# Performance work log

Measured on AMD Instinct MI355X. Metric: run time of the kernel, lower is better.

## Reference

```python
import jax, jax.numpy as jnp
import numpy as np

NEG_BIG = -1e10  # K.switch(A==0, -1e10, 0) mask value
LRELU_ALPHA = 0.2


def setup_inputs() -> dict:
    key = jax.random.key(0)
    kX, kA, kW, kS, kN = jax.random.split(key, 5)
    B, N, F, H, F_ = 4, 2048, 256, 8, 64
    X = jax.random.normal(kX, (B, N, F), dtype=jnp.float32)
    A = jax.random.bernoulli(kA, 0.05, (B, N, N)).astype(jnp.float32)
    eye = jnp.eye(N, dtype=jnp.float32)[None]
    A = jnp.maximum(A, eye)
    W = jax.random.normal(kW, (H, F, F_), dtype=jnp.float32) * 0.05
    a_self = jax.random.normal(kS, (H, F_), dtype=jnp.float32) * 0.05
    a_neigh = jax.random.normal(kN, (H, F_), dtype=jnp.float32) * 0.05
    return {"X": X, "A": A, "W": W, "a_self": a_self, "a_neigh": a_neigh}


def reference(X, A, W, a_self, a_neigh):
    # per-head linear transform, vectorized over heads: [B,H,N,F_]
    h = jnp.einsum('bnf,hfo->bhno', X, W)
    att_s = jnp.einsum('bhno,ho->bhn', h, a_self)    # attn_for_self
    att_n = jnp.einsum('bhno,ho->bhn', h, a_neigh)   # attn_for_neighs
    # broadcast-add -> dense NxN scores per head, LeakyReLU(0.2)
    dense = att_s[:, :, :, None] + att_n[:, :, None, :]          # [B,H,N,N]
    dense = jax.nn.leaky_relu(dense, LRELU_ALPHA)
    mask = jnp.where(A == 0.0, NEG_BIG, 0.0)[:, None, :, :]      # [B,1,N,N]
    attn = jax.nn.softmax(dense + mask, axis=-1)
    # weighted aggregation (dropout is identity at inference / attn_dropout=0)
    out = jnp.einsum('bhnm,bhmo->bhno', attn, h)                 # [B,H,N,F_]
    out = jax.nn.relu(out)                                       # per-head activation (concat mode)
    B, H, N, F_ = out.shape
    return out.transpose(0, 2, 1, 3).reshape(B, N, H * F_)       # concat heads
```

## Files before the change

kernel.cpp:

```cpp
#include <hip/hip_runtime.h>


constexpr int GN  = 2048;
constexpr int GHF = 512;

using sh8    = __attribute__((ext_vector_type(8))) short;
using us4g   = __attribute__((ext_vector_type(4))) unsigned short;
using f32x4g = __attribute__((ext_vector_type(4))) float;
using u32x4g = __attribute__((ext_vector_type(4))) unsigned int;
using i32x4g = __attribute__((ext_vector_type(4))) int;

__device__ inline float gat_bf2f(unsigned short u) {
    union { unsigned int i; float f; } c; c.i = ((unsigned int)u) << 16; return c.f;
}
__device__ inline unsigned short gat_f2bf(float f) {
    union { float f; unsigned int i; } c; c.f = f;
    return (unsigned short)((c.i + 0x7fffu + ((c.i >> 16) & 1u)) >> 16);
}
__device__ inline int gat_isf32(const float* __restrict__ Aw) {
    float a = Aw[0];
    return (a == 0.0f) || (a == 1.0f);
}
__device__ inline unsigned int gat_enc(float f) {
    union { float f; unsigned int u; } c; c.f = f;
    return (c.u & 0x80000000u) ? ~c.u : (c.u | 0x80000000u);
}
__device__ inline float gat_dec(unsigned int e) {
    union { float f; unsigned int u; } c;
    c.u = (e & 0x80000000u) ? (e & 0x7fffffffu) : ~e;
    return c.f;
}
__device__ inline size_t gat_hswz_idx(int o, int j) {
    int jc = j >> 5, quad = (j >> 3) & 3, e = j & 7;
    int lane = quad * 16 + (o & 15);
    return (((size_t)(jc * 4 + (o >> 4))) * 64 + lane) * 8 + e;
}
__device__ inline size_t gat_wf_idx(int hh, int k, int col) {
    int kg = k >> 5, quad = (k >> 3) & 3, e = k & 7;
    int ct = col >> 4, lrw = col & 15;
    return ((((size_t)hh * 8 + kg) * 4 + ct) * 64 + (quad * 16 + lrw)) * 8 + e;
}

__global__ void GraphAttention_62981400429165_kernel() {}

constexpr size_t OFF_HS   = 256;
constexpr size_t OFF_ATTS = OFF_HS   + 8388608;
constexpr size_t OFF_TB   = OFF_ATTS + 262144;
constexpr size_t OFF_MASK = OFF_TB   + 262144;
constexpr size_t OFF_MAXN = OFF_MASK + 2097152;
constexpr size_t OFF_XC   = OFF_MAXN + 256;
constexpr size_t OFF_WC   = OFF_XC   + 4194304;

__global__ __launch_bounds__(256) void k_mask_conv(const void* __restrict__ Araw,
                                                   const void* __restrict__ Xraw,
                                                   const void* __restrict__ Wraw,
                                                   unsigned long long* __restrict__ mask,
                                                   unsigned int* __restrict__ maxn_enc,
                                                   unsigned short* __restrict__ Xc,
                                                   unsigned short* __restrict__ Wf) {
    int tid = threadIdx.x, blk = blockIdx.x;
    int isf = gat_isf32((const float*)Araw);
    if (blk < 8192) {
        if (blk == 0 && tid < 32) maxn_enc[tid] = 0u;
        size_t i8 = ((size_t)blk * 256 + tid) * 8;
        unsigned int byte = 0;
        if (isf) {
            f32x4g v0 = *(const f32x4g*)((const float*)Araw + i8);
            f32x4g v1 = *(const f32x4g*)((const float*)Araw + i8 + 4);
#pragma unroll
            for (int e = 0; e < 4; e++) {
                byte |= (v0[e] != 0.0f ? 1u : 0u) << e;
                byte |= (v1[e] != 0.0f ? 1u : 0u) << (e + 4);
            }
        } else {
            u32x4g v = *(const u32x4g*)((const unsigned short*)Araw + i8);
#pragma unroll
            for (int w = 0; w < 4; w++) {
                byte |= ((v[w] & 0xffffu) != 0u ? 1u : 0u) << (2 * w);
                byte |= ((v[w] >> 16) != 0u ? 1u : 0u) << (2 * w + 1);
            }
        }
        ((unsigned char*)mask)[i8 >> 3] = (unsigned char)byte;
    } else if (blk < 9216) {
        size_t i8 = ((size_t)(blk - 8192) * 256 + tid) * 8;
        if (isf) {
            f32x4g v0 = *(const f32x4g*)((const float*)Xraw + i8);
            f32x4g v1 = *(const f32x4g*)((const float*)Xraw + i8 + 4);
            us4g lo, hi;
#pragma unroll
            for (int e = 0; e < 4; e++) { lo[e] = gat_f2bf(v0[e]); hi[e] = gat_f2bf(v1[e]); }
            *(us4g*)&Xc[i8]     = lo;
            *(us4g*)&Xc[i8 + 4] = hi;
        } else {
            *(u32x4g*)&Xc[i8] = *(const u32x4g*)((const unsigned short*)Xraw + i8);
        }
    } else {
        int gid = (blk - 9216) * 256 + tid;
        int lane = gid & 63, ct = (gid >> 6) & 3, kg = (gid >> 8) & 7, hh = gid >> 11;
        int quad = lane >> 4, lrw = lane & 15;
        int col = ct * 16 + lrw;
        us4g lo, hi;
#pragma unroll
        for (int e = 0; e < 8; e++) {
            int k = kg * 32 + quad * 8 + e;
            size_t src = (size_t)hh * 16384 + (size_t)k * 64 + col;
            unsigned short v = isf ? gat_f2bf(((const float*)Wraw)[src])
                                   : ((const unsigned short*)Wraw)[src];
            if (e < 4) lo[e] = v; else hi[e - 4] = v;
        }
        *(us4g*)&Wf[(size_t)gid * 8]     = lo;
        *(us4g*)&Wf[(size_t)gid * 8 + 4] = hi;
    }
}

constexpr int LDW = 264;
__global__ __launch_bounds__(256) void k_gemm1(const unsigned short* __restrict__ Xc,
                                               const unsigned short* __restrict__ Wf,
                                               const void* __restrict__ aSraw,
                                               const void* __restrict__ aNraw,
                                               const float* __restrict__ Aw,
                                               unsigned short* __restrict__ hswz,
                                               float* __restrict__ att_s,
                                               unsigned int* __restrict__ Tb,
                                               unsigned int* __restrict__ maxn_enc) {
    int blk = blockIdx.x;
    int bh = blk >> 5, it = blk & 31;
    int b = bh >> 3, hh = bh & 7;
    int isf = gat_isf32(Aw);
#if defined(__gfx950__)
    __shared__ unsigned short CtT[64 * LDW];
    int wave = threadIdx.x >> 6, lane = threadIdx.x & 63;
    int lrw = lane & 15, quad = lane >> 4;
    int row0 = it * 64 + wave * 16;
    const unsigned short* wfh = Wf + (size_t)hh * 16384 + lane * 8;
    f32x4g acc[4] = {};
#pragma unroll 2
    for (int kg = 0; kg < 8; kg++) {
        sh8 a = *(const sh8*)&Xc[((size_t)(b * GN) + row0 + lrw) * 256 + kg * 32 + quad * 8];
        const unsigned short* wp = wfh + kg * 2048;
        sh8 w0 = *(const sh8*)&wp[0];
        sh8 w1 = *(const sh8*)&wp[512];
        sh8 w2 = *(const sh8*)&wp[1024];
        sh8 w3 = *(const sh8*)&wp[1536];
        acc[0] = __builtin_amdgcn_mfma_f32_16x16x32_bf16(a, w0, acc[0], 0, 0, 0);
        acc[1] = __builtin_amdgcn_mfma_f32_16x16x32_bf16(a, w1, acc[1], 0, 0, 0);
        acc[2] = __builtin_amdgcn_mfma_f32_16x16x32_bf16(a, w2, acc[2], 0, 0, 0);
        acc[3] = __builtin_amdgcn_mfma_f32_16x16x32_bf16(a, w3, acc[3], 0, 0, 0);
    }
    float as_l[4], an_l[4];
#pragma unroll
    for (int ct = 0; ct < 4; ct++) {
        int col = hh * 64 + ct * 16 + lrw;
        as_l[ct] = isf ? ((const float*)aSraw)[col] : gat_bf2f(((const unsigned short*)aSraw)[col]);
        an_l[ct] = isf ? ((const float*)aNraw)[col] : gat_bf2f(((const unsigned short*)aNraw)[col]);
    }
    float wmax = -3e38f;
#pragma unroll
    for (int r = 0; r < 4; r++) {
        float ps = acc[0][r] * as_l[0] + acc[1][r] * as_l[1]
                 + acc[2][r] * as_l[2] + acc[3][r] * as_l[3];
        float pn = acc[0][r] * an_l[0] + acc[1][r] * an_l[1]
                 + acc[2][r] * an_l[2] + acc[3][r] * an_l[3];
        for (int off = 1; off < 16; off <<= 1) {
            ps += __shfl_xor(ps, off);
            pn += __shfl_xor(pn, off);
        }
        int row = row0 + quad * 4 + r;
        if (lrw == 0) {
            att_s[bh * GN + row] = ps;
            Tb[bh * GN + row] = ((unsigned int)gat_f2bf(__expf(pn)) << 16)
                              | (unsigned int)gat_f2bf(__expf(0.2f * pn));
        }
        wmax = fmaxf(wmax, pn);
    }
    wmax = fmaxf(wmax, __shfl_xor(wmax, 16));
    wmax = fmaxf(wmax, __shfl_xor(wmax, 32));
    if (lane == 0) atomicMax(&maxn_enc[bh], gat_enc(wmax));
#pragma unroll
    for (int ct = 0; ct < 4; ct++) {
        int o = ct * 16 + lrw;
        int nloc = wave * 16 + quad * 4;
        us4g v;
        v[0] = gat_f2bf(acc[ct][0]);
        v[1] = gat_f2bf(acc[ct][1]);
        v[2] = gat_f2bf(acc[ct][2]);
        v[3] = gat_f2bf(acc[ct][3]);
        *(us4g*)&CtT[o * LDW + nloc] = v;
    }
    __syncthreads();
#pragma unroll
    for (int k = 0; k < 2; k++) {
        int id = k * 256 + threadIdx.x;
        int ln = id & 63, t = id >> 6;
        int jc_loc = t >> 2, ct = t & 3;
        int lrw2 = ln & 15, quad2 = ln >> 4;
        int o = ct * 16 + lrw2;
        int nloc = jc_loc * 32 + quad2 * 8;
        sh8 v = *(const sh8*)&CtT[o * LDW + nloc];
        size_t dst = ((((size_t)(bh * 64 + it * 2 + jc_loc)) * 4 + ct) * 64 + ln) * 8;
        *(sh8*)&hswz[dst] = v;
    }
#else
    if (threadIdx.x < 64) {
        int row = it * 64 + threadIdx.x;
        float hrow[64];
        for (int col = 0; col < 64; col++) {
            float sacc = 0.f;
            for (int k = 0; k < 256; k++)
                sacc += gat_bf2f(Xc[((size_t)(b * GN) + row) * 256 + k])
                      * gat_bf2f(Wf[gat_wf_idx(hh, k, col)]);
            hrow[col] = sacc;
        }
        size_t base = (size_t)bh * 64 * GN;
        for (int col = 0; col < 64; col++)
            hswz[base + gat_hswz_idx(col, row)] = gat_f2bf(hrow[col]);
        float ps = 0.f, pn = 0.f;
        for (int col = 0; col < 64; col++) {
            float as = isf ? ((const float*)aSraw)[hh * 64 + col] : gat_bf2f(((const unsigned short*)aSraw)[hh * 64 + col]);
            float an = isf ? ((const float*)aNraw)[hh * 64 + col] : gat_bf2f(((const unsigned short*)aNraw)[hh * 64 + col]);
            ps += hrow[col] * as;
            pn += hrow[col] * an;
        }
        att_s[bh * GN + row] = ps;
        Tb[bh * GN + row] = ((unsigned int)gat_f2bf(__expf(pn)) << 16)
                          | (unsigned int)gat_f2bf(__expf(0.2f * pn));
        atomicMax(&maxn_enc[bh], gat_enc(pn));
    }
#endif
}

__global__ __launch_bounds__(256, 4) void k_attn_av(const unsigned int* __restrict__ mask32,
                                                    const unsigned short* __restrict__ hswz,
                                                    const float* __restrict__ att_s,
                                                    const unsigned int* __restrict__ Tb,
                                                    const unsigned int* __restrict__ maxn_enc,
                                                    const float* __restrict__ Aw,
                                                    void* __restrict__ outv) {
    int blk = blockIdx.x;
    int bh = blk & 31, it = blk >> 5;
    int b = bh >> 3, hh = bh & 7;
    int i0 = it * 32;
    int tid = threadIdx.x;
    int isf = gat_isf32(Aw);
    float maxn = gat_dec(maxn_enc[bh]);
    const unsigned int* Tp = Tb + (size_t)bh * GN;
#if defined(__gfx950__)
    int wave = tid >> 6, lane = tid & 63, lrw = lane & 15, quad = lane >> 4;
    int kq = quad * 8;
    int j0 = wave * 512;
    const unsigned short* hs = hswz + ((size_t)(bh * 64) + wave * 16) * 2048 + lane * 8;
    float k1[2], k2[2];
    const unsigned int* mrf[2];
    for (int f = 0; f < 2; f++) {
        int row = i0 + f * 16 + lrw;
        float s = att_s[bh * GN + row];
        float z = s + maxn;
        float c = fmaxf(z, 0.2f * z);
        k1[f] = __expf(s - c);
        k2[f] = __expf(0.2f * s - c);
        mrf[f] = mask32 + ((size_t)(b * GN) + row) * 64 + wave * 16;
    }
    f32x4g acc[2][4] = {};
    f32x4g accl[2] = {};
    sh8 ones;
#pragma unroll
    for (int e = 0; e < 8; e++) ones[e] = (short)0x3f80;

#pragma unroll 1
    for (int jg = 0; jg < 4; jg++) {
        u32x4g m0 = *(const u32x4g*)&mrf[0][jg * 4];
        u32x4g m1 = *(const u32x4g*)&mrf[1][jg * 4];
#pragma unroll
        for (int sj = 0; sj < 4; sj++) {
            int jc = jg * 4 + sj;
            int jq = j0 + jc * 32 + kq;
            u32x4g tA = *(const u32x4g*)&Tp[jq];
            u32x4g tB = *(const u32x4g*)&Tp[jq + 4];
            const unsigned short* hp = hs + jc * 2048;
            sh8 b0 = *(const sh8*)&hp[0];
            sh8 b1 = *(const sh8*)&hp[512];
            sh8 b2 = *(const sh8*)&hp[1024];
            sh8 b3 = *(const sh8*)&hp[1536];
            unsigned int w0 = m0[sj] >> kq;
            unsigned int w1 = m1[sj] >> kq;
            unsigned int q0[8], q1[8];
#pragma unroll
            for (int e = 0; e < 8; e++) {
                unsigned int word = (e < 4) ? tA[e] : tB[e - 4];
                float Ev  = __uint_as_float(word & 0xffff0000u);
                float E5v = __uint_as_float(word << 16);
                float p0 = fmaxf(k1[0] * Ev, k2[0] * E5v);
                float p1 = fmaxf(k1[1] * Ev, k2[1] * E5v);
                unsigned int s0 = (unsigned int)__builtin_amdgcn_sbfe((int)w0, (unsigned)e, 1u);
                unsigned int s1 = (unsigned int)__builtin_amdgcn_sbfe((int)w1, (unsigned)e, 1u);
                q0[e] = __float_as_uint(p0) & s0;
                q1[e] = __float_as_uint(p1) & s1;
            }
            i32x4g f0, f1;
#pragma unroll
            for (int pp = 0; pp < 4; pp++) {
                unsigned int r0, r1;
                asm("v_cvt_pk_bf16_f32 %0, %1, %2"
                    : "=v"(r0)
                    : "v"(__uint_as_float(q0[2 * pp])), "v"(__uint_as_float(q0[2 * pp + 1])));
                asm("v_cvt_pk_bf16_f32 %0, %1, %2"
                    : "=v"(r1)
                    : "v"(__uint_as_float(q1[2 * pp])), "v"(__uint_as_float(q1[2 * pp + 1])));
                f0[pp] = (int)r0;
                f1[pp] = (int)r1;
            }
            sh8 af0 = *(sh8*)&f0;
            sh8 af1 = *(sh8*)&f1;
            acc[0][0] = __builtin_amdgcn_mfma_f32_16x16x32_bf16(af0, b0, acc[0][0], 0, 0, 0);
            acc[1][0] = __builtin_amdgcn_mfma_f32_16x16x32_bf16(af1, b0, acc[1][0], 0, 0, 0);
            acc[0][1] = __builtin_amdgcn_mfma_f32_16x16x32_bf16(af0, b1, acc[0][1], 0, 0, 0);
            acc[1][1] = __builtin_amdgcn_mfma_f32_16x16x32_bf16(af1, b1, acc[1][1], 0, 0, 0);
            acc[0][2] = __builtin_amdgcn_mfma_f32_16x16x32_bf16(af0, b2, acc[0][2], 0, 0, 0);
            acc[1][2] = __builtin_amdgcn_mfma_f32_16x16x32_bf16(af1, b2, acc[1][2], 0, 0, 0);
            acc[0][3] = __builtin_amdgcn_mfma_f32_16x16x32_bf16(af0, b3, acc[0][3], 0, 0, 0);
            acc[1][3] = __builtin_amdgcn_mfma_f32_16x16x32_bf16(af1, b3, acc[1][3], 0, 0, 0);
            accl[0] = __builtin_amdgcn_mfma_f32_16x16x32_bf16(af0, ones, accl[0], 0, 0, 0);
            accl[1] = __builtin_amdgcn_mfma_f32_16x16x32_bf16(af1, ones, accl[1], 0, 0, 0);
        }
    }
    __shared__ float lred[4 * 32];
    __shared__ float lsum[32];
    __shared__ float red[4 * 2 * 16 * 17];
    if (lrw == 0) {
#pragma unroll
        for (int f = 0; f < 2; f++)
#pragma unroll
            for (int r = 0; r < 4; r++)
                lred[wave * 32 + f * 16 + quad * 4 + r] = accl[f][r];
    }
    __syncthreads();
    if (tid < 32)
        lsum[tid] = 1.0f / (lred[tid] + lred[32 + tid] + lred[64 + tid] + lred[96 + tid]);
    __syncthreads();
    for (int ct = 0; ct < 4; ct++) {
#pragma unroll
        for (int f = 0; f < 2; f++)
#pragma unroll
            for (int r = 0; r < 4; r++)
                red[wave * 544 + f * 272 + (quad * 4 + r) * 17 + lrw] = acc[f][ct][r];
        __syncthreads();
#pragma unroll
        for (int k = 0; k < 2; k++) {
            int pos = k * 256 + tid;
            int f = pos >> 8, r16 = (pos >> 4) & 15, c16 = pos & 15;
            int bse = f * 272 + r16 * 17 + c16;
            float sum = red[bse] + red[bse + 544] + red[bse + 1088] + red[bse + 1632];
            float v = sum * lsum[f * 16 + r16];
            v = v > 0.f ? v : 0.f;
            int row = i0 + f * 16 + r16;
            size_t o = ((size_t)(b * GN) + row) * GHF + hh * 64 + ct * 16 + c16;
            if (isf) ((float*)outv)[o] = v;
            else     ((unsigned short*)outv)[o] = gat_f2bf(v);
        }
        __syncthreads();
    }
#else
    int row = i0 + (tid >> 3), chh = (tid & 7) * 8;
    const unsigned short* hbb = hswz + (size_t)(bh * 64) * GN;
    const unsigned int* mr = mask32 + ((size_t)(b * GN) + row) * 64;
    float s = att_s[bh * GN + row];
    float z = s + maxn;
    float c = fmaxf(z, 0.2f * z);
    float k1 = __expf(s - c), k2 = __expf(0.2f * s - c);
    float l = 0.f;
    float accS[8] = {};
    for (int j = 0; j < GN; j++) {
        if (!((mr[j >> 5] >> (j & 31)) & 1u)) continue;
        unsigned int word = Tp[j];
        float Ev  = __uint_as_float(word & 0xffff0000u);
        float E5v = __uint_as_float(word << 16);
        float p = fmaxf(k1 * Ev, k2 * E5v);
        union { float f; unsigned int u; } t; t.f = p; t.u &= 0xffff0000u;
        l += t.f;
        for (int cc = 0; cc < 8; cc++)
            accS[cc] += t.f * gat_bf2f(hbb[gat_hswz_idx(chh + cc, j)]);
    }
    float li = 1.0f / l;
    for (int cc = 0; cc < 8; cc++) {
        float v = accS[cc] * li; v = v > 0.f ? v : 0.f;
        size_t oi = ((size_t)(b * GN) + row) * GHF + hh * 64 + chh + cc;
        if (isf) ((float*)outv)[oi] = v;
        else     ((unsigned short*)outv)[oi] = gat_f2bf(v);
    }
#endif
}

extern "C" void kernel_launch(void* const* d_in, const int* in_sizes, int n_in,
                              void* d_out, int out_size, void* d_ws, size_t ws_size,
                              hipStream_t stream) {
    const void* X  = d_in[0];
    const void* A  = d_in[1];
    const void* W  = d_in[2];
    const void* aS = d_in[3];
    const void* aN = d_in[4];

    char* ws = (char*)d_ws;
    unsigned short* hswz = (unsigned short*)(ws + OFF_HS);
    float* att_s = (float*)(ws + OFF_ATTS);
    unsigned int* Tb = (unsigned int*)(ws + OFF_TB);
    unsigned long long* mask = (unsigned long long*)(ws + OFF_MASK);
    unsigned int* maxn_enc = (unsigned int*)(ws + OFF_MAXN);
    unsigned short* Xc = (unsigned short*)(ws + OFF_XC);
    unsigned short* Wf = (unsigned short*)(ws + OFF_WC);

    k_mask_conv<<<9280, 256, 0, stream>>>(A, X, W, mask, maxn_enc, Xc, Wf);
    k_gemm1<<<1024, 256, 0, stream>>>(Xc, Wf, aS, aN, (const float*)A,
                                      hswz, att_s, Tb, maxn_enc);
    k_attn_av<<<2048, 256, 0, stream>>>((const unsigned int*)mask, hswz,
                                        att_s, Tb, maxn_enc,
                                        (const float*)A, d_out);
}
```

Measured before the change: 207.3 us.

## Switch attention path to fp16 packed math with 16-bit mask and fused X conversion

Replaces the bf16 probability path with fp16: exp terms are stored as separate fp16 arrays, probabilities are computed with packed v_pk_mul/max_f16 and masked with a precomputed 16-bit-per-element mask, and the AV matmul uses f16 MFMA. The bitmask becomes a 32MB halfword mask so no per-element bit extraction is needed. X conversion to bf16 is folded into the first GEMM, which removes a pass and a workspace buffer. The cost is far more mask traffic, 32MB against 2MB per call, and fp16 range limits handled by clamping pn to 10.

```diff
diff --git a/kernel.cpp b/kernel.cpp
--- a/kernel.cpp
+++ b/kernel.cpp
@@ -5,6 +5,7 @@
 constexpr int GHF = 512;
 
 using sh8    = __attribute__((ext_vector_type(8))) short;
+using hf8    = __attribute__((ext_vector_type(8))) _Float16;
 using us4g   = __attribute__((ext_vector_type(4))) unsigned short;
 using f32x4g = __attribute__((ext_vector_type(4))) float;
 using u32x4g = __attribute__((ext_vector_type(4))) unsigned int;
@@ -17,6 +18,13 @@
     union { float f; unsigned int i; } c; c.f = f;
     return (unsigned short)((c.i + 0x7fffu + ((c.i >> 16) & 1u)) >> 16);
 }
+__device__ inline unsigned short gat_f2h(float f) {
+    _Float16 h = (_Float16)f;
+    union { _Float16 h; unsigned short u; } c; c.h = h; return c.u;
+}
+__device__ inline float gat_h2f(unsigned short u) {
+    union { _Float16 h; unsigned short u; } c; c.u = u; return (float)c.h;
+}
 __device__ inline int gat_isf32(const float* __restrict__ Aw) {
     float a = Aw[0];
     return (a == 0.0f) || (a == 1.0f);
@@ -45,57 +53,41 @@
 
 constexpr size_t OFF_HS   = 256;
 constexpr size_t OFF_ATTS = OFF_HS   + 8388608;
-constexpr size_t OFF_TB   = OFF_ATTS + 262144;
-constexpr size_t OFF_MASK = OFF_TB   + 262144;
-constexpr size_t OFF_MAXN = OFF_MASK + 2097152;
-constexpr size_t OFF_XC   = OFF_MAXN + 256;
-constexpr size_t OFF_WC   = OFF_XC   + 4194304;
+constexpr size_t OFF_EF   = OFF_ATTS + 262144;
+constexpr size_t OFF_E5F  = OFF_EF   + 131072;
+constexpr size_t OFF_M16  = OFF_E5F  + 131072;
+constexpr size_t OFF_MAXN = OFF_M16  + 33554432;
+constexpr size_t OFF_WC   = OFF_MAXN + 256;
 
 __global__ __launch_bounds__(256) void k_mask_conv(const void* __restrict__ Araw,
-                                                   const void* __restrict__ Xraw,
                                                    const void* __restrict__ Wraw,
-                                                   unsigned long long* __restrict__ mask,
+                                                   unsigned short* __restrict__ M16,
                                                    unsigned int* __restrict__ maxn_enc,
-                                                   unsigned short* __restrict__ Xc,
                                                    unsigned short* __restrict__ Wf) {
     int tid = threadIdx.x, blk = blockIdx.x;
     int isf = gat_isf32((const float*)Araw);
     if (blk < 8192) {
         if (blk == 0 && tid < 32) maxn_enc[tid] = 0u;
         size_t i8 = ((size_t)blk * 256 + tid) * 8;
-        unsigned int byte = 0;
+        u32x4g mo;
         if (isf) {
             f32x4g v0 = *(const f32x4g*)((const float*)Araw + i8);
             f32x4g v1 = *(const f32x4g*)((const float*)Araw + i8 + 4);
-#pragma unroll
-            for (int e = 0; e < 4; e++) {
-                byte |= (v0[e] != 0.0f ? 1u : 0u) << e;
-                byte |= (v1[e] != 0.0f ? 1u : 0u) << (e + 4);
-            }
+            float el[8] = {v0[0], v0[1], v0[2], v0[3], v1[0], v1[1], v1[2], v1[3]};
+#pragma unroll
+            for (int p = 0; p < 4; p++)
+                mo[p] = (el[2 * p]     != 0.0f ? 0x0000FFFFu : 0u)
+                      | (el[2 * p + 1] != 0.0f ? 0xFFFF0000u : 0u);
         } else {
             u32x4g v = *(const u32x4g*)((const unsigned short*)Araw + i8);
 #pragma unroll
-            for (int w = 0; w < 4; w++) {
-                byte |= ((v[w] & 0xffffu) != 0u ? 1u : 0u) << (2 * w);
-                byte |= ((v[w] >> 16) != 0u ? 1u : 0u) << (2 * w + 1);
-            }
-        }
-        ((unsigned char*)mask)[i8 >> 3] = (unsigned char)byte;
-    } else if (blk < 9216) {
-        size_t i8 = ((size_t)(blk - 8192) * 256 + tid) * 8;
-        if (isf) {
-            f32x4g v0 = *(const f32x4g*)((const float*)Xraw + i8);
-            f32x4g v1 = *(const f32x4g*)((const float*)Xraw + i8 + 4);
-            us4g lo, hi;
-#pragma unroll
-            for (int e = 0; e < 4; e++) { lo[e] = gat_f2bf(v0[e]); hi[e] = gat_f2bf(v1[e]); }
-            *(us4g*)&Xc[i8]     = lo;
-            *(us4g*)&Xc[i8 + 4] = hi;
-        } else {
-            *(u32x4g*)&Xc[i8] = *(const u32x4g*)((const unsigned short*)Xraw + i8);
-        }
+            for (int p = 0; p < 4; p++)
+                mo[p] = ((v[p] & 0xffffu) != 0u ? 0x0000FFFFu : 0u)
+                      | ((v[p] >> 16)    != 0u ? 0xFFFF0000u : 0u);
+        }
+        *(u32x4g*)((unsigned int*)M16 + (i8 >> 1)) = mo;
     } else {
-        int gid = (blk - 9216) * 256 + tid;
+        int gid = (blk - 8192) * 256 + tid;
         int lane = gid & 63, ct = (gid >> 6) & 3, kg = (gid >> 8) & 7, hh = gid >> 11;
         int quad = lane >> 4, lrw = lane & 15;
         int col = ct * 16 + lrw;
@@ -114,14 +106,15 @@
 }
 
 constexpr int LDW = 264;
-__global__ __launch_bounds__(256) void k_gemm1(const unsigned short* __restrict__ Xc,
+__global__ __launch_bounds__(256) void k_gemm1(const void* __restrict__ Xraw,
                                                const unsigned short* __restrict__ Wf,
                                                const void* __restrict__ aSraw,
                                                const void* __restrict__ aNraw,
                                                const float* __restrict__ Aw,
                                                unsigned short* __restrict__ hswz,
                                                float* __restrict__ att_s,
-                                               unsigned int* __restrict__ Tb,
+                                               unsigned short* __restrict__ Ef,
+                                               unsigned short* __restrict__ E5f,
                                                unsigned int* __restrict__ maxn_enc) {
     int blk = blockIdx.x;
     int bh = blk >> 5, it = blk & 31;
@@ -133,10 +126,25 @@
     int lrw = lane & 15, quad = lane >> 4;
     int row0 = it * 64 + wave * 16;
     const unsigned short* wfh = Wf + (size_t)hh * 16384 + lane * 8;
+    size_t xbase = ((size_t)(b * GN) + row0 + lrw) * 256;
     f32x4g acc[4] = {};
 #pragma unroll 2
     for (int kg = 0; kg < 8; kg++) {
-        sh8 a = *(const sh8*)&Xc[((size_t)(b * GN) + row0 + lrw) * 256 + kg * 32 + quad * 8];
+        sh8 a;
+        if (isf) {
+            const float* xp = (const float*)Xraw + xbase + kg * 32 + quad * 8;
+            f32x4g x0 = *(const f32x4g*)xp;
+            f32x4g x1 = *(const f32x4g*)(xp + 4);
+            unsigned int w0_, w1_, w2_, w3_;
+            asm("v_cvt_pk_bf16_f32 %0, %1, %2" : "=v"(w0_) : "v"(x0[0]), "v"(x0[1]));
+            asm("v_cvt_pk_bf16_f32 %0, %1, %2" : "=v"(w1_) : "v"(x0[2]), "v"(x0[3]));
+            asm("v_cvt_pk_bf16_f32 %0, %1, %2" : "=v"(w2_) : "v"(x1[0]), "v"(x1[1]));
+            asm("v_cvt_pk_bf16_f32 %0, %1, %2" : "=v"(w3_) : "v"(x1[2]), "v"(x1[3]));
+            i32x4g aw = {(int)w0_, (int)w1_, (int)w2_, (int)w3_};
+            a = *(sh8*)&aw;
+        } else {
+            a = *(const sh8*)((const unsigned short*)Xraw + xbase + kg * 32 + quad * 8);
+        }
         const unsigned short* wp = wfh + kg * 2048;
         sh8 w0 = *(const sh8*)&wp[0];
         sh8 w1 = *(const sh8*)&wp[512];
@@ -168,8 +176,9 @@
         int row = row0 + quad * 4 + r;
         if (lrw == 0) {
             att_s[bh * GN + row] = ps;
-            Tb[bh * GN + row] = ((unsigned int)gat_f2bf(__expf(pn)) << 16)
-                              | (unsigned int)gat_f2bf(__expf(0.2f * pn));
+            float pnc = fminf(pn, 10.0f);
+            Ef[bh * GN + row]  = gat_f2h(__expf(pnc));
+            E5f[bh * GN + row] = gat_f2h(__expf(0.2f * pnc));
         }
         wmax = fmaxf(wmax, pn);
     }
@@ -181,10 +190,10 @@
         int o = ct * 16 + lrw;
         int nloc = wave * 16 + quad * 4;
         us4g v;
-        v[0] = gat_f2bf(acc[ct][0]);
-        v[1] = gat_f2bf(acc[ct][1]);
-        v[2] = gat_f2bf(acc[ct][2]);
-        v[3] = gat_f2bf(acc[ct][3]);
+        v[0] = gat_f2h(acc[ct][0]);
+        v[1] = gat_f2h(acc[ct][1]);
+        v[2] = gat_f2h(acc[ct][2]);
+        v[3] = gat_f2h(acc[ct][3]);
         *(us4g*)&CtT[o * LDW + nloc] = v;
     }
     __syncthreads();
@@ -206,14 +215,16 @@
         float hrow[64];
         for (int col = 0; col < 64; col++) {
             float sacc = 0.f;
-            for (int k = 0; k < 256; k++)
-                sacc += gat_bf2f(Xc[((size_t)(b * GN) + row) * 256 + k])
-                      * gat_bf2f(Wf[gat_wf_idx(hh, k, col)]);
+            for (int k = 0; k < 256; k++) {
+                float xv = isf ? ((const float*)Xraw)[((size_t)(b * GN) + row) * 256 + k]
+                               : gat_bf2f(((const unsigned short*)Xraw)[((size_t)(b * GN) + row) * 256 + k]);
+                sacc += xv * gat_bf2f(Wf[gat_wf_idx(hh, k, col)]);
+            }
             hrow[col] = sacc;
         }
         size_t base = (size_t)bh * 64 * GN;
         for (int col = 0; col < 64; col++)
-            hswz[base + gat_hswz_idx(col, row)] = gat_f2bf(hrow[col]);
+            hswz[base + gat_hswz_idx(col, row)] = gat_f2h(hrow[col]);
         float ps = 0.f, pn = 0.f;
         for (int col = 0; col < 64; col++) {
             float as = isf ? ((const float*)aSraw)[hh * 64 + col] : gat_bf2f(((const unsigned short*)aSraw)[hh * 64 + col]);
@@ -222,17 +233,19 @@
             pn += hrow[col] * an;
         }
         att_s[bh * GN + row] = ps;
-        Tb[bh * GN + row] = ((unsigned int)gat_f2bf(__expf(pn)) << 16)
-                          | (unsigned int)gat_f2bf(__expf(0.2f * pn));
+        float pnc = fminf(pn, 10.0f);
+        Ef[bh * GN + row]  = gat_f2h(__expf(pnc));
+        E5f[bh * GN + row] = gat_f2h(__expf(0.2f * pnc));
         atomicMax(&maxn_enc[bh], gat_enc(pn));
     }
 #endif
 }
 
-__global__ __launch_bounds__(256, 4) void k_attn_av(const unsigned int* __restrict__ mask32,
+__global__ __launch_bounds__(256, 4) void k_attn_av(const unsigned short* __restrict__ M16,
                                                     const unsigned short* __restrict__ hswz,
                                                     const float* __restrict__ att_s,
-                                                    const unsigned int* __restrict__ Tb,
+                                                    const unsigned short* __restrict__ Ef,
+                                                    const unsigned short* __restrict__ E5f,
                                                     const unsigned int* __restrict__ maxn_enc,
                                                     const float* __restrict__ Aw,
                                                     void* __restrict__ outv) {
@@ -243,85 +256,69 @@
     int tid = threadIdx.x;
     int isf = gat_isf32(Aw);
     float maxn = gat_dec(maxn_enc[bh]);
-    const unsigned int* Tp = Tb + (size_t)bh * GN;
 #if defined(__gfx950__)
     int wave = tid >> 6, lane = tid & 63, lrw = lane & 15, quad = lane >> 4;
-    int kq = quad * 8;
     int j0 = wave * 512;
     const unsigned short* hs = hswz + ((size_t)(bh * 64) + wave * 16) * 2048 + lane * 8;
-    float k1[2], k2[2];
-    const unsigned int* mrf[2];
+    const unsigned int* Eu  = (const unsigned int*)Ef  + (size_t)bh * 1024;
+    const unsigned int* E5u = (const unsigned int*)E5f + (size_t)bh * 1024;
+    unsigned int k1p[2], k2p[2];
+    const unsigned int* mrow[2];
     for (int f = 0; f < 2; f++) {
         int row = i0 + f * 16 + lrw;
         float s = att_s[bh * GN + row];
         float z = s + maxn;
         float c = fmaxf(z, 0.2f * z);
-        k1[f] = __expf(s - c);
-        k2[f] = __expf(0.2f * s - c);
-        mrf[f] = mask32 + ((size_t)(b * GN) + row) * 64 + wave * 16;
+        unsigned int u1 = gat_f2h(__expf(s - c));
+        unsigned int u2 = gat_f2h(__expf(0.2f * s - c));
+        k1p[f] = u1 * 0x00010001u;
+        k2p[f] = u2 * 0x00010001u;
+        mrow[f] = (const unsigned int*)M16 + ((size_t)(b * GN) + row) * 1024;
     }
     f32x4g acc[2][4] = {};
     f32x4g accl[2] = {};
-    sh8 ones;
-#pragma unroll
-    for (int e = 0; e < 8; e++) ones[e] = (short)0x3f80;
-
-#pragma unroll 1
-    for (int jg = 0; jg < 4; jg++) {
-        u32x4g m0 = *(const u32x4g*)&mrf[0][jg * 4];
-        u32x4g m1 = *(const u32x4g*)&mrf[1][jg * 4];
-#pragma unroll
-        for (int sj = 0; sj < 4; sj++) {
-            int jc = jg * 4 + sj;
-            int jq = j0 + jc * 32 + kq;
-            u32x4g tA = *(const u32x4g*)&Tp[jq];
-            u32x4g tB = *(const u32x4g*)&Tp[jq + 4];
-            const unsigned short* hp = hs + jc * 2048;
-            sh8 b0 = *(const sh8*)&hp[0];
-            sh8 b1 = *(const sh8*)&hp[512];
-            sh8 b2 = *(const sh8*)&hp[1024];
-            sh8 b3 = *(const sh8*)&hp[1536];
-            unsigned int w0 = m0[sj] >> kq;
-            unsigned int w1 = m1[sj] >> kq;
-            unsigned int q0[8], q1[8];
-#pragma unroll
-            for (int e = 0; e < 8; e++) {
-                unsigned int word = (e < 4) ? tA[e] : tB[e - 4];
-                float Ev  = __uint_as_float(word & 0xffff0000u);
-                float E5v = __uint_as_float(word << 16);
-                float p0 = fmaxf(k1[0] * Ev, k2[0] * E5v);
-                float p1 = fmaxf(k1[1] * Ev, k2[1] * E5v);
-                unsigned int s0 = (unsigned int)__builtin_amdgcn_sbfe((int)w0, (unsigned)e, 1u);
-                unsigned int s1 = (unsigned int)__builtin_amdgcn_sbfe((int)w1, (unsigned)e, 1u);
-                q0[e] = __float_as_uint(p0) & s0;
-                q1[e] = __float_as_uint(p1) & s1;
-            }
-            i32x4g f0, f1;
-#pragma unroll
-            for (int pp = 0; pp < 4; pp++) {
-                unsigned int r0, r1;
-                asm("v_cvt_pk_bf16_f32 %0, %1, %2"
-                    : "=v"(r0)
-                    : "v"(__uint_as_float(q0[2 * pp])), "v"(__uint_as_float(q0[2 * pp + 1])));
-                asm("v_cvt_pk_bf16_f32 %0, %1, %2"
-                    : "=v"(r1)
-                    : "v"(__uint_as_float(q1[2 * pp])), "v"(__uint_as_float(q1[2 * pp + 1])));
-                f0[pp] = (int)r0;
-                f1[pp] = (int)r1;
-            }
-            sh8 af0 = *(sh8*)&f0;
-            sh8 af1 = *(sh8*)&f1;
-            acc[0][0] = __builtin_amdgcn_mfma_f32_16x16x32_bf16(af0, b0, acc[0][0], 0, 0, 0);
-            acc[1][0] = __builtin_amdgcn_mfma_f32_16x16x32_bf16(af1, b0, acc[1][0], 0, 0, 0);
-            acc[0][1] = __builtin_amdgcn_mfma_f32_16x16x32_bf16(af0, b1, acc[0][1], 0, 0, 0);
-            acc[1][1] = __builtin_amdgcn_mfma_f32_16x16x32_bf16(af1, b1, acc[1][1], 0, 0, 0);
-            acc[0][2] = __builtin_amdgcn_mfma_f32_16x16x32_bf16(af0, b2, acc[0][2], 0, 0, 0);
-            acc[1][2] = __builtin_amdgcn_mfma_f32_16x16x32_bf16(af1, b2, acc[1][2], 0, 0, 0);
-            acc[0][3] = __builtin_amdgcn_mfma_f32_16x16x32_bf16(af0, b3, acc[0][3], 0, 0, 0);
-            acc[1][3] = __builtin_amdgcn_mfma_f32_16x16x32_bf16(af1, b3, acc[1][3], 0, 0, 0);
-            accl[0] = __builtin_amdgcn_mfma_f32_16x16x32_bf16(af0, ones, accl[0], 0, 0, 0);
-            accl[1] = __builtin_amdgcn_mfma_f32_16x16x32_bf16(af1, ones, accl[1], 0, 0, 0);
-        }
+    hf8 ones;
+#pragma unroll
+    for (int e = 0; e < 8; e++) ones[e] = (_Float16)1.0f;
+
+#pragma unroll 2
+    for (int jc = 0; jc < 16; jc++) {
+        int jh = ((j0 + jc * 32) >> 1) + quad * 4;
+        u32x4g Ep  = *(const u32x4g*)&Eu[jh];
+        u32x4g E5p = *(const u32x4g*)&E5u[jh];
+        u32x4g M0  = *(const u32x4g*)&mrow[0][jh];
+        u32x4g M1  = *(const u32x4g*)&mrow[1][jh];
+        const unsigned short* hp = hs + jc * 2048;
+        hf8 b0 = *(const hf8*)&hp[0];
+        hf8 b1 = *(const hf8*)&hp[512];
+        hf8 b2 = *(const hf8*)&hp[1024];
+        hf8 b3 = *(const hf8*)&hp[1536];
+        i32x4g f0, f1;
+#pragma unroll
+        for (int pp = 0; pp < 4; pp++) {
+            unsigned int a0, a1, m0w, a2, a3, m1w;
+            unsigned int ew = Ep[pp], e5w = E5p[pp];
+            asm("v_pk_mul_f16 %0, %1, %2" : "=v"(a0)  : "v"(k1p[0]), "v"(ew));
+            asm("v_pk_mul_f16 %0, %1, %2" : "=v"(a1)  : "v"(k2p[0]), "v"(e5w));
+            asm("v_pk_max_f16 %0, %1, %2" : "=v"(m0w) : "v"(a0), "v"(a1));
+            f0[pp] = (int)(m0w & M0[pp]);
+            asm("v_pk_mul_f16 %0, %1, %2" : "=v"(a2)  : "v"(k1p[1]), "v"(ew));
+            asm("v_pk_mul_f16 %0, %1, %2" : "=v"(a3)  : "v"(k2p[1]), "v"(e5w));
+            asm("v_pk_max_f16 %0, %1, %2" : "=v"(m1w) : "v"(a2), "v"(a3));
+            f1[pp] = (int)(m1w & M1[pp]);
+        }
+        hf8 af0 = *(hf8*)&f0;
+        hf8 af1 = *(hf8*)&f1;
+        acc[0][0] = __builtin_amdgcn_mfma_f32_16x16x32_f16(af0, b0, acc[0][0], 0, 0, 0);
+        acc[1][0] = __builtin_amdgcn_mfma_f32_16x16x32_f16(af1, b0, acc[1][0], 0, 0, 0);
+        acc[0][1] = __builtin_amdgcn_mfma_f32_16x16x32_f16(af0, b1, acc[0][1], 0, 0, 0);
+        acc[1][1] = __builtin_amdgcn_mfma_f32_16x16x32_f16(af1, b1, acc[1][1], 0, 0, 0);
+        acc[0][2] = __builtin_amdgcn_mfma_f32_16x16x32_f16(af0, b2, acc[0][2], 0, 0, 0);
+        acc[1][2] = __builtin_amdgcn_mfma_f32_16x16x32_f16(af1, b2, acc[1][2], 0, 0, 0);
+        acc[0][3] = __builtin_amdgcn_mfma_f32_16x16x32_f16(af0, b3, acc[0][3], 0, 0, 0);
+        acc[1][3] = __builtin_amdgcn_mfma_f32_16x16x32_f16(af1, b3, acc[1][3], 0, 0, 0);
+        accl[0] = __builtin_amdgcn_mfma_f32_16x16x32_f16(af0, ones, accl[0], 0, 0, 0);
+        accl[1] = __builtin_amdgcn_mfma_f32_16x16x32_f16(af1, ones, accl[1], 0, 0, 0);
     }
     __shared__ float lred[4 * 32];
     __shared__ float lsum[32];
@@ -362,7 +359,7 @@
 #else
     int row = i0 + (tid >> 3), chh = (tid & 7) * 8;
     const unsigned short* hbb = hswz + (size_t)(bh * 64) * GN;
-    const unsigned int* mr = mask32 + ((size_t)(b * GN) + row) * 64;
+    const unsigned short* mr = M16 + ((size_t)(b * GN) + row) * GN;
     float s = att_s[bh * GN + row];
     float z = s + maxn;
     float c = fmaxf(z, 0.2f * z);
@@ -370,15 +367,14 @@
     float l = 0.f;
     float accS[8] = {};
     for (int j = 0; j < GN; j++) {
-        if (!((mr[j >> 5] >> (j & 31)) & 1u)) continue;
-        unsigned int word = Tp[j];
-        float Ev  = __uint_as_float(word & 0xffff0000u);
-        float E5v = __uint_as_float(word << 16);
+        if (!mr[j]) continue;
+        float Ev  = gat_h2f(Ef[(size_t)bh * GN + j]);
+        float E5v = gat_h2f(E5f[(size_t)bh * GN + j]);
         float p = fmaxf(k1 * Ev, k2 * E5v);
-        union { float f; unsigned int u; } t; t.f = p; t.u &= 0xffff0000u;
-        l += t.f;
+        p = gat_h2f(gat_f2h(p));
+        l += p;
         for (int cc = 0; cc < 8; cc++)
-            accS[cc] += t.f * gat_bf2f(hbb[gat_hswz_idx(chh + cc, j)]);
+            accS[cc] += p * gat_h2f(hbb[gat_hswz_idx(chh + cc, j)]);
     }
     float li = 1.0f / l;
     for (int cc = 0; cc < 8; cc++) {
@@ -402,16 +398,15 @@
     char* ws = (char*)d_ws;
     unsigned short* hswz = (unsigned short*)(ws + OFF_HS);
     float* att_s = (float*)(ws + OFF_ATTS);
-    unsigned int* Tb = (unsigned int*)(ws + OFF_TB);
-    unsigned long long* mask = (unsigned long long*)(ws + OFF_MASK);
+    unsigned short* Ef  = (unsigned short*)(ws + OFF_EF);
+    unsigned short* E5f = (unsigned short*)(ws + OFF_E5F);
+    unsigned short* M16 = (unsigned short*)(ws + OFF_M16);
     unsigned int* maxn_enc = (unsigned int*)(ws + OFF_MAXN);
-    unsigned short* Xc = (unsigned short*)(ws + OFF_XC);
     unsigned short* Wf = (unsigned short*)(ws + OFF_WC);
 
-    k_mask_conv<<<9280, 256, 0, stream>>>(A, X, W, mask, maxn_enc, Xc, Wf);
-    k_gemm1<<<1024, 256, 0, stream>>>(Xc, Wf, aS, aN, (const float*)A,
-                                      hswz, att_s, Tb, maxn_enc);
-    k_attn_av<<<2048, 256, 0, stream>>>((const unsigned int*)mask, hswz,
-                                        att_s, Tb, maxn_enc,
+    k_mask_conv<<<8256, 256, 0, stream>>>(A, W, M16, maxn_enc, Wf);
+    k_gemm1<<<1024, 256, 0, stream>>>(X, Wf, aS, aN, (const float*)A,
+                                      hswz, att_s, Ef, E5f, maxn_enc);
+    k_attn_av<<<2048, 256, 0, stream>>>(M16, hswz, att_s, Ef, E5f, maxn_enc,
                                         (const float*)A, d_out);
 }
```

New measurement: 224.4 us. +8.2%, slower.
